# Kernel tuning notes

Hardware: AMD Instinct MI355X
Metric: run time of the kernel (lower is better)

Reference implementation:

```python
import jax, jax.numpy as jnp
from jax import lax
import numpy as np

B, T, K = 512, 512, 64


def setup_inputs() -> dict:
    key = jax.random.key(0)
    k1, k2, k3, k4 = jax.random.split(key, 4)
    return {
        "emissions": jax.random.normal(k1, (B, T, K), dtype=jnp.float32),
        "attn_mask": jnp.ones((B, T), dtype=jnp.int32),
        "start_transitions": jax.random.normal(k2, (K,), dtype=jnp.float32) * 0.1,
        "end_transitions": jax.random.normal(k3, (K,), dtype=jnp.float32) * 0.1,
        "transitions": jax.random.normal(k4, (K, K), dtype=jnp.float32) * 0.1,
    }


def reference(emissions, attn_mask, start_transitions, end_transitions, transitions):
    """Viterbi decode (torchcrf CRF.decode). Returns best tag paths [B, T] int32."""
    mask = attn_mask.astype(bool)  # [B, T]; mask[:, 0] assumed all True (torchcrf requirement)
    score0 = start_transitions[None, :] + emissions[:, 0]  # [B, K]

    emits = jnp.swapaxes(emissions[:, 1:], 0, 1)  # [T-1, B, K]
    masks = jnp.swapaxes(mask[:, 1:], 0, 1)       # [T-1, B]

    def viterbi_step(score, xs):
        emit_t, mask_t = xs                                        # [B,K], [B]
        cand = score[:, :, None] + transitions[None, :, :] + emit_t[:, None, :]  # [B,Kprev,Knext]
        next_score = cand.max(axis=1)                              # [B, K]
        idx = cand.argmax(axis=1).astype(jnp.int32)                # [B, K] best prev tag
        new_score = jnp.where(mask_t[:, None], next_score, score)  # freeze past seq end
        return new_score, idx

    final_score, history = lax.scan(viterbi_step, score0, (emits, masks))
    final_score = final_score + end_transitions[None, :]           # [B, K]
    best_last = jnp.argmax(final_score, axis=1).astype(jnp.int32)  # [B]

    def backtrace_step(tag, xs):
        idx_t, mask_t = xs  # [B, K], [B]
        prev = jnp.take_along_axis(idx_t, tag[:, None], axis=1)[:, 0]
        new_tag = jnp.where(mask_t, prev, tag)
        return new_tag, new_tag

    _, tags_prefix = lax.scan(backtrace_step, best_last, (history, masks), reverse=True)
    tags = jnp.concatenate([tags_prefix, best_last[None, :]], axis=0)  # [T, B]
    return jnp.swapaxes(tags, 0, 1)  # [B, T]
```

## Files before the change

### kernel.cpp

```cpp
#include <hip/hip_runtime.h>
#include <hip/hip_bf16.h>


#define TT 512
#define BB 512
#define KK 64
#define NW 4
#define IW 16

#define NEG_INF (-3.402823466e38f)

__global__ __launch_bounds__(256) void viterbi_fwd(
    const float* __restrict__ emissions,
    const int* __restrict__ attn_mask,
    const float* __restrict__ start_t,
    const float* __restrict__ end_t,
    const float* __restrict__ trans,
    unsigned char* __restrict__ hist,
    int* __restrict__ best_last)
{
    const int b   = blockIdx.x;
    const int tid = threadIdx.x;
    const int j   = tid & 63;
    const int w   = __builtin_amdgcn_readfirstlane(tid >> 6);
    const int iwb = w * IW;

    __shared__ float vbuf[2][NW][KK];
    __shared__ int   ibuf[2][NW][KK];

    float tc[IW];
#pragma unroll
    for (int q = 0; q < IW; ++q) tc[q] = trans[(iwb + q) * KK + j];

    const float* eb = emissions + (size_t)b * TT * KK;
    const int*   mb = attn_mask + (size_t)b * TT;
    unsigned char* hb = hist + (size_t)b * TT * KK;

    float score = start_t[j] + eb[j];

    float e0 = eb[KK + j];
    float e1 = eb[2 * KK + j];
    int   m0 = mb[1];
    int   m1 = mb[2];

    for (int t = 1; t < TT; ++t) {
        float e = e0; e0 = e1;
        int   m = m0; m0 = m1;
        int tn = (t + 2 < TT) ? (t + 2) : (TT - 1);
        e1 = eb[(size_t)tn * KK + j];
        m1 = mb[tn];

        float b0 = NEG_INF, b1 = NEG_INF;
        int   i0 = iwb,     i1 = iwb + 8;
#pragma unroll
        for (int q = 0; q < 8; ++q) {
            float s0 = __uint_as_float(
                __builtin_amdgcn_readlane(__float_as_uint(score), iwb + q));
            float c0 = (s0 + tc[q]) + e;
            if (c0 > b0) { b0 = c0; i0 = iwb + q; }

            float s1 = __uint_as_float(
                __builtin_amdgcn_readlane(__float_as_uint(score), iwb + 8 + q));
            float c1 = (s1 + tc[8 + q]) + e;
            if (c1 > b1) { b1 = c1; i1 = iwb + 8 + q; }
        }
        float bw = b0; int iw_ = i0;
        if (b1 > bw) { bw = b1; iw_ = i1; }

        const int p = t & 1;
        vbuf[p][w][j] = bw;
        ibuf[p][w][j] = iw_;
        __syncthreads();

        float best = vbuf[p][0][j]; int bi = ibuf[p][0][j];
        {
            float v = vbuf[p][1][j]; int q_ = ibuf[p][1][j];
            if (v > best) { best = v; bi = q_; }
            v = vbuf[p][2][j]; q_ = ibuf[p][2][j];
            if (v > best) { best = v; bi = q_; }
            v = vbuf[p][3][j]; q_ = ibuf[p][3][j];
            if (v > best) { best = v; bi = q_; }
        }

        if (w == 0) hb[(size_t)(t - 1) * KK + j] = (unsigned char)bi;
        score = m ? best : score;
    }

    float fin = score + end_t[j];
    __syncthreads();
    if (w == 0) vbuf[0][0][j] = fin;
    __syncthreads();
    if (tid == 0) {
        float bv = vbuf[0][0][0]; int bt = 0;
#pragma unroll
        for (int k = 1; k < KK; ++k) {
            float v = vbuf[0][0][k];
            if (v > bv) { bv = v; bt = k; }
        }
        best_last[b] = bt;
    }
}

__global__ __launch_bounds__(64) void viterbi_bt(
    const unsigned char* __restrict__ hist,
    const int* __restrict__ attn_mask,
    const int* __restrict__ best_last,
    int* __restrict__ out)
{
    const int b = blockIdx.x;
    const int l = threadIdx.x;
    __shared__ int path[TT];

    const unsigned int* hw = (const unsigned int*)(hist + (size_t)b * TT * KK);
    const int* mb = attn_mask + (size_t)b * TT;

    int tag = best_last[b];
    if (l == 0) path[TT - 1] = tag;

    unsigned int dwA[16], dwB[16];
    int mA, mB;

    auto loadChunk = [&](int c, unsigned int (&dw)[16], int& mreg) {
#pragma unroll
        for (int q4 = 0; q4 < 16; ++q4)
            dw[q4] = hw[c * 1024 + q4 * 64 + l];
        int midx = c * 64 + l + 1;
        if (midx > TT - 1) midx = TT - 1;
        mreg = mb[midx];
    };
    auto procChunk = [&](int c, unsigned int (&dw)[16], int mreg) {
#pragma unroll
        for (int q = 63; q >= 0; --q) {
            int r = c * 64 + q;
            if (r < TT - 1) {
                unsigned int d = __shfl(dw[q >> 2], ((q & 3) << 4) + (tag >> 2));
                int pv = (int)((d >> ((tag & 3) << 3)) & 0xFFu);
                int m  = __shfl(mreg, q);
                tag = m ? pv : tag;
                if (l == 0) path[r] = tag;
            }
        }
    };

    loadChunk(7, dwA, mA);
    for (int c = 7; c >= 1; c -= 2) {
        loadChunk(c - 1, dwB, mB);
        procChunk(c, dwA, mA);
        if (c >= 2) loadChunk(c - 2, dwA, mA);
        procChunk(c - 1, dwB, mB);
    }

    __syncthreads();
#pragma unroll
    for (int cc = 0; cc < 8; ++cc)
        out[(size_t)b * TT + cc * 64 + l] = path[cc * 64 + l];
}

extern "C" void kernel_launch(void* const* d_in, const int* in_sizes, int n_in,
                              void* d_out, int out_size, void* d_ws, size_t ws_size,
                              hipStream_t stream) {
    const float* emissions = (const float*)d_in[0];
    const int* attn_mask   = (const int*)d_in[1];
    const float* start_t   = (const float*)d_in[2];
    const float* end_t     = (const float*)d_in[3];
    const float* trans     = (const float*)d_in[4];
    int* out = (int*)d_out;

    unsigned char* hist = (unsigned char*)d_ws;
    int* best_last = (int*)((char*)d_ws + (size_t)BB * TT * KK);

    viterbi_fwd<<<BB, NW * KK, 0, stream>>>(emissions, attn_mask, start_t, end_t,
                                            trans, hist, best_last);
    viterbi_bt<<<BB, KK, 0, stream>>>(hist, attn_mask, best_last, out);
}
```

Before: 464.0 us.

## Use one wavefront per sequence in Viterbi forward, removing per-step block barriers

The forward kernel moves from four wavefronts per sequence, each covering 16 previous tags and merging through shared memory with a __syncthreads every step, to a single 64-lane wavefront per sequence. Each lane now keeps all 64 transition values in registers and runs 8 groups of 8 readlane-based max/argmax, then merges the groups. This removes the per-timestep shared-memory exchange and barrier. In exchange each thread does four times the serial compare work per step, uses more registers, and the block count stays at 512 with only one wave each.

```diff
diff --git a/kernel.cpp b/kernel.cpp
--- a/kernel.cpp
+++ b/kernel.cpp
@@ -5,12 +5,10 @@
 #define TT 512
 #define BB 512
 #define KK 64
-#define NW 4
-#define IW 16
 
 #define NEG_INF (-3.402823466e38f)
 
-__global__ __launch_bounds__(256) void viterbi_fwd(
+__global__ __launch_bounds__(64) void viterbi_fwd(
     const float* __restrict__ emissions,
     const int* __restrict__ attn_mask,
     const float* __restrict__ start_t,
@@ -19,18 +17,12 @@
     unsigned char* __restrict__ hist,
     int* __restrict__ best_last)
 {
-    const int b   = blockIdx.x;
-    const int tid = threadIdx.x;
-    const int j   = tid & 63;
-    const int w   = __builtin_amdgcn_readfirstlane(tid >> 6);
-    const int iwb = w * IW;
+    const int b = blockIdx.x;
+    const int j = threadIdx.x & 63;
 
-    __shared__ float vbuf[2][NW][KK];
-    __shared__ int   ibuf[2][NW][KK];
-
-    float tc[IW];
+    float tc[KK];
 #pragma unroll
-    for (int q = 0; q < IW; ++q) tc[q] = trans[(iwb + q) * KK + j];
+    for (int i = 0; i < KK; ++i) tc[i] = trans[i * KK + j];
 
     const float* eb = emissions + (size_t)b * TT * KK;
     const int*   mb = attn_mask + (size_t)b * TT;
@@ -50,51 +42,45 @@
         e1 = eb[(size_t)tn * KK + j];
         m1 = mb[tn];
 
-        float b0 = NEG_INF, b1 = NEG_INF;
-        int   i0 = iwb,     i1 = iwb + 8;
+        float gv[8];
+        int   gi[8];
 #pragma unroll
-        for (int q = 0; q < 8; ++q) {
+        for (int g = 0; g < 8; ++g) {
+            const int base = g * 8;
             float s0 = __uint_as_float(
-                __builtin_amdgcn_readlane(__float_as_uint(score), iwb + q));
-            float c0 = (s0 + tc[q]) + e;
-            if (c0 > b0) { b0 = c0; i0 = iwb + q; }
+                __builtin_amdgcn_readlane(__float_as_uint(score), base));
+            float bv = (s0 + tc[base]) + e;
+            int   bi = base;
+#pragma unroll
+            for (int q = 1; q < 8; ++q) {
+                float s = __uint_as_float(
+                    __builtin_amdgcn_readlane(__float_as_uint(score), base + q));
+                float c = (s + tc[base + q]) + e;
+                if (c > bv) { bv = c; bi = base + q; }
+            }
+            gv[g] = bv;
+            gi[g] = bi;
+        }
+        float best = gv[0];
+        int   bi   = gi[0];
+#pragma unroll
+        for (int g = 1; g < 8; ++g)
+            if (gv[g] > best) { best = gv[g]; bi = gi[g]; }
 
-            float s1 = __uint_as_float(
-                __builtin_amdgcn_readlane(__float_as_uint(score), iwb + 8 + q));
-            float c1 = (s1 + tc[8 + q]) + e;
-            if (c1 > b1) { b1 = c1; i1 = iwb + 8 + q; }
-        }
-        float bw = b0; int iw_ = i0;
-        if (b1 > bw) { bw = b1; iw_ = i1; }
-
-        const int p = t & 1;
-        vbuf[p][w][j] = bw;
-        ibuf[p][w][j] = iw_;
-        __syncthreads();
-
-        float best = vbuf[p][0][j]; int bi = ibuf[p][0][j];
-        {
-            float v = vbuf[p][1][j]; int q_ = ibuf[p][1][j];
-            if (v > best) { best = v; bi = q_; }
-            v = vbuf[p][2][j]; q_ = ibuf[p][2][j];
-            if (v > best) { best = v; bi = q_; }
-            v = vbuf[p][3][j]; q_ = ibuf[p][3][j];
-            if (v > best) { best = v; bi = q_; }
-        }
-
-        if (w == 0) hb[(size_t)(t - 1) * KK + j] = (unsigned char)bi;
+        hb[(size_t)(t - 1) * KK + j] = (unsigned char)bi;
         score = m ? best : score;
     }
 
     float fin = score + end_t[j];
+    __shared__ float sv[KK];
+    sv[j] = fin;
     __syncthreads();
-    if (w == 0) vbuf[0][0][j] = fin;
-    __syncthreads();
-    if (tid == 0) {
-        float bv = vbuf[0][0][0]; int bt = 0;
+    if (j == 0) {
+        float bv = sv[0];
+        int   bt = 0;
 #pragma unroll
         for (int k = 1; k < KK; ++k) {
-            float v = vbuf[0][0][k];
+            float v = sv[k];
             if (v > bv) { bv = v; bt = k; }
         }
         best_last[b] = bt;
@@ -169,7 +155,7 @@
     unsigned char* hist = (unsigned char*)d_ws;
     int* best_last = (int*)((char*)d_ws + (size_t)BB * TT * KK);
 
-    viterbi_fwd<<<BB, NW * KK, 0, stream>>>(emissions, attn_mask, start_t, end_t,
-                                            trans, hist, best_last);
+    viterbi_fwd<<<BB, KK, 0, stream>>>(emissions, attn_mask, start_t, end_t,
+                                       trans, hist, best_last);
     viterbi_bt<<<BB, KK, 0, stream>>>(hist, attn_mask, best_last, out);
 }
```

New measurement: 624.6 us. 1.35x slower.
